# Kernel tuning notes

Measured on AMD Instinct MI355X. Metric: run time of the kernel, lower is better.

## Reference

```python
import jax, jax.numpy as jnp
import numpy as np

E = 8       # n_experts
K = 2       # k_experts
D_IN = 1024
D_OUT = 1024
D_EXP = 2048
N = 16384   # tokens (batch*seq, forward requires 2D input)


def setup_inputs() -> dict:
    key = jax.random.key(0)
    ks = jax.random.split(key, 4)
    x = jax.random.normal(ks[0], (N, D_IN), jnp.float32)
    Wg = jax.random.normal(ks[1], (E, D_IN), jnp.float32) * 0.02      # router weight
    bg = jnp.zeros((E,), jnp.float32)                                  # router bias
    W_in = jax.random.normal(ks[2], (E, D_EXP, D_IN), jnp.float32) * 0.02
    b_in = jnp.zeros((E, D_EXP), jnp.float32)                          # w_in_bias_init=0.0
    W_out = jax.random.normal(ks[3], (E, D_OUT, D_EXP), jnp.float32) * 0.02  # bias=False
    return {"x": x, "Wg": Wg, "bg": bg, "W_in": W_in, "b_in": b_in, "W_out": W_out}


def moe_forward(x, Wg, bg, W_in, b_in, W_out):
    # Eval mode: gate jitter / solu jitter / dropouts are training-only no-ops.
    n = x.shape[0]
    # --- routing ---
    logits = x @ Wg.T + bg                                 # [N, E]
    probs = jax.nn.softmax(logits, axis=-1)
    mean_probs = probs.mean(axis=0)                        # [E]
    k_vals, k_idx = jax.lax.top_k(probs, K)                # [N, K]
    k_w = k_vals / k_vals.sum(axis=-1, keepdims=True)      # renormalized gate weights
    counts = jnp.bincount(k_idx.reshape(-1), length=E)     # [E] int
    load_balancing_loss = E * jnp.sum((counts.astype(x.dtype) / n) * mean_probs)
    # --- dispatch + expert w_in (loop over fixed small E; combine with one-hot mask) ---
    sel = jax.nn.one_hot(k_idx, E, dtype=x.dtype)          # [N, K, E]
    h = jnp.zeros((n, K, D_EXP), x.dtype)                  # preacts per (token, slot)
    for e in range(E):
        he = x @ W_in[e].T + b_in[e]                       # [N, D_EXP]
        h = h + sel[:, :, e][..., None] * he[:, None, :]
    # --- SoLU (eval): softmax(preacts) * preacts over hidden dim ---
    acts = jax.nn.softmax(h, axis=-1) * h                  # [N, K, D_EXP]
    # --- expert w_out (no bias) ---
    out = jnp.zeros((n, K, D_OUT), x.dtype)
    for e in range(E):
        oe = jnp.einsum('nkh,oh->nko', acts, W_out[e])
        out = out + sel[:, :, e][..., None] * oe
    # --- weighted combine over the K chosen experts ---
    outputs = (out * k_w[..., None]).sum(axis=1)           # [N, D_OUT]
    return outputs, load_balancing_loss


def reference(x, Wg, bg, W_in, b_in, W_out):
    return moe_forward(x, Wg, bg, W_in, b_in, W_out)
```

## Files before the change

### kernel.cpp

```cpp
#include <hip/hip_runtime.h>
#include <hip/hip_bf16.h>
#include <stdint.h>

#define E_EXP 8
#define NTOK  16384
#define DIN   1024
#define DEXP  2048
#define DOUT  1024
#define NSLOT (NTOK*2)
#define MAXT  136

#define TS_T  (256*64)

typedef __attribute__((ext_vector_type(8))) short short8;
typedef __attribute__((ext_vector_type(8))) unsigned short ushort8;
typedef __attribute__((ext_vector_type(4))) unsigned short ushort4v;
typedef __attribute__((ext_vector_type(4))) float f32x4;

__device__ __forceinline__ unsigned short f2bf(float f){
  union { float f; uint32_t u; } v; v.f = f;
  uint32_t r = (v.u + 0x7FFFu + ((v.u >> 16) & 1u)) >> 16;
  return (unsigned short)r;
}
__device__ __forceinline__ float bf2f(unsigned short u){
  union { uint32_t u; float f; } v; v.u = ((uint32_t)u) << 16;
  return v.f;
}

__device__ __forceinline__ void async16(const void* g, void* l){
  __builtin_amdgcn_global_load_lds(
      (const __attribute__((address_space(1))) void*)g,
      (__attribute__((address_space(3))) void*)l, 16, 0, 0);
}

#define VMCNT8()  asm volatile("s_waitcnt vmcnt(8)"  ::: "memory")
#define VMCNT0()  asm volatile("s_waitcnt vmcnt(0)"  ::: "memory")
#define BARRIER() do { asm volatile("" ::: "memory"); __builtin_amdgcn_s_barrier(); asm volatile("" ::: "memory"); } while(0)

__global__ __launch_bounds__(256) void cast2(const float* __restrict__ a,
                                             const float* __restrict__ b,
                                             unsigned short* __restrict__ da,
                                             unsigned short* __restrict__ db,
                                             int na, int nb){
  int i = (blockIdx.x*256 + threadIdx.x)*8;
  const float* s; unsigned short* d;
  if (i < na){ s = a + i; d = da + i; }
  else { int j = i - na; if (j >= nb) return; s = b + j; d = db + j; }
  float4 x = *(const float4*)(s);
  float4 y = *(const float4*)(s+4);
  ushort8 o;
  o[0]=f2bf(x.x); o[1]=f2bf(x.y); o[2]=f2bf(x.z); o[3]=f2bf(x.w);
  o[4]=f2bf(y.x); o[5]=f2bf(y.y); o[6]=f2bf(y.z); o[7]=f2bf(y.w);
  *(ushort8*)d = o;
}

__global__ __launch_bounds__(256) void router(
    const float* __restrict__ x, const float* __restrict__ Wg, const float* __restrict__ bg,
    unsigned short* __restrict__ xb,
    int* __restrict__ eidx, float* __restrict__ gw,
    int* __restrict__ counts, float* __restrict__ probsum)
{
  __shared__ float sWg[E_EXP*DIN];
  __shared__ float sps[E_EXP];
  __shared__ int   scnt[E_EXP];
  const int tid = threadIdx.x;
  for (int i = tid; i < E_EXP*DIN; i += 256) sWg[i] = Wg[i];
  if (tid < E_EXP){ sps[tid]=0.f; scnt[tid]=0; }
  __syncthreads();
  const int lane = tid & 63;
  const int wv   = tid >> 6;
  for (int it = 0; it < 16; ++it){
    const int token = blockIdx.x*64 + wv*16 + it;
    float4 xv[4];
#pragma unroll
    for (int j=0;j<4;++j) xv[j] = *(const float4*)&x[(size_t)token*DIN + j*256 + lane*4];
#pragma unroll
    for (int j=0;j<4;++j){
      ushort4v o;
      o[0]=f2bf(xv[j].x); o[1]=f2bf(xv[j].y); o[2]=f2bf(xv[j].z); o[3]=f2bf(xv[j].w);
      *(ushort4v*)&xb[(size_t)token*DIN + j*256 + lane*4] = o;
    }
    float p[E_EXP];
#pragma unroll
    for (int e2=0;e2<E_EXP;++e2){
      float s = 0.f;
#pragma unroll
      for (int j=0;j<4;++j){
        const float4 w4 = *(const float4*)&sWg[e2*DIN + j*256 + lane*4];
        s += xv[j].x*w4.x + xv[j].y*w4.y + xv[j].z*w4.z + xv[j].w*w4.w;
      }
      p[e2] = s;
    }
#pragma unroll
    for (int d=1; d<64; d<<=1){
#pragma unroll
      for (int e2=0;e2<E_EXP;++e2) p[e2] += __shfl_xor(p[e2], d);
    }
    if (lane == 0){
      float mx = -1e30f;
#pragma unroll
      for (int e2=0;e2<E_EXP;++e2){ p[e2] += bg[e2]; mx = fmaxf(mx, p[e2]); }
      float se = 0.f;
#pragma unroll
      for (int e2=0;e2<E_EXP;++e2){ p[e2] = __expf(p[e2]-mx); se += p[e2]; }
      const float inv = 1.f/se;
#pragma unroll
      for (int e2=0;e2<E_EXP;++e2){ p[e2] *= inv; atomicAdd(&sps[e2], p[e2]); }
      int i1 = 0;
#pragma unroll
      for (int e2=1;e2<E_EXP;++e2) if (p[e2] > p[i1]) i1 = e2;
      int i2 = (i1==0) ? 1 : 0;
#pragma unroll
      for (int e2=0;e2<E_EXP;++e2) if (e2 != i1 && p[e2] > p[i2]) i2 = e2;
      const float v1 = p[i1], v2 = p[i2], s12 = v1 + v2;
      eidx[2*token]   = i1; eidx[2*token+1] = i2;
      gw[2*token]     = v1/s12; gw[2*token+1] = v2/s12;
      atomicAdd(&scnt[i1], 1); atomicAdd(&scnt[i2], 1);
    }
  }
  __syncthreads();
  if (tid < E_EXP){ atomicAdd(&counts[tid], scnt[tid]); atomicAdd(&probsum[tid], sps[tid]); }
}

__global__ void finalize(const int* __restrict__ counts, const float* __restrict__ probsum,
                         float* __restrict__ loss_out, int* __restrict__ offs,
                         int* __restrict__ cursor, int* __restrict__ tile_e,
                         int* __restrict__ tile_row, int* __restrict__ ntiles)
{
  const int lane = threadIdx.x;
  int c[E_EXP];
#pragma unroll
  for (int e=0;e<E_EXP;++e) c[e] = counts[e];
  int off[E_EXP+1], tb[E_EXP+1];
  off[0]=0; tb[0]=0;
#pragma unroll
  for (int e=0;e<E_EXP;++e){ off[e+1]=off[e]+c[e]; tb[e+1]=tb[e]+((c[e]+255)>>8); }
  if (lane==0){
    float loss=0.f;
#pragma unroll
    for (int e=0;e<E_EXP;++e) loss += (float)c[e]*probsum[e];
    *loss_out = loss * (8.f/((float)NTOK*(float)NTOK));
    *ntiles = tb[E_EXP];
    offs[E_EXP] = off[E_EXP];
  }
  if (lane < E_EXP){ cursor[lane]=0; offs[lane]=off[lane]; }
  const int nt = tb[E_EXP];
  for (int i=lane; i<nt; i+=64){
    int e=0;
#pragma unroll
    for (int k=0;k<E_EXP-1;++k) if (i >= tb[k+1]) e = k+1;
    tile_e[i]   = e;
    tile_row[i] = off[e] + (i - tb[e])*256;
  }
}

__global__ __launch_bounds__(256) void scatter(const int* __restrict__ eidx,
    const int* __restrict__ offs, int* __restrict__ cursor,
    int* __restrict__ ptok, int* __restrict__ inv)
{
  const int t = blockIdx.x*256 + threadIdx.x;
  if (t >= NTOK) return;
#pragma unroll
  for (int s=0;s<2;++s){
    const int e2  = eidx[2*t+s];
    const int pos = offs[e2] + atomicAdd(&cursor[e2], 1);
    ptok[pos] = t;
    inv[2*t+s] = pos;
  }
}

__global__ __launch_bounds__(512) void gemm1(
    const unsigned short* __restrict__ xb,
    const unsigned short* __restrict__ wib,
    const float* __restrict__ b_in,
    unsigned short* __restrict__ H,
    const int* __restrict__ ptok,
    const int* __restrict__ offs,
    const int* __restrict__ tile_e,
    const int* __restrict__ tile_row,
    const int* __restrict__ ntiles)
{
  const int gid   = (int)blockIdx.y * 8 + (int)blockIdx.x;
  const int rank  = (gid & 7) * 136 + (gid >> 3);
  const int rtile = rank >> 3;
  const int panel = rank & 7;
  if (rtile >= *ntiles) return;
  const int e    = tile_e[rtile];
  const int row0 = tile_row[rtile];
  const int seg_end = offs[e+1];
  const int col0 = panel * 256;

  __shared__ unsigned short As[2][TS_T];
  __shared__ unsigned short Bs[2][TS_T];

  const int tid  = threadIdx.x;
  const int lane = tid & 63;
  const int wv   = tid >> 6;
  const int wm   = wv >> 2;
  const int wn   = wv & 3;
  const int srow = tid >> 3;
  const int scol = ((tid & 7) ^ (srow & 7)) * 8;

  const unsigned short* ag[4];
#pragma unroll
  for (int i = 0; i < 4; ++i){
    int g = row0 + i*64 + srow; if (g > NSLOT-1) g = NSLOT-1;
    const int tok = ptok[g];
    ag[i] = xb + (size_t)tok*DIN + scol;
  }
  const unsigned short* bg4[4];
#pragma unroll
  for (int i = 0; i < 4; ++i)
    bg4[i] = wib + ((size_t)e*DEXP + col0 + i*64 + srow)*DIN + scol;
  float bias[4];
#pragma unroll
  for (int n = 0; n < 4; ++n)
    bias[n] = b_in[e*DEXP + col0 + wn*64 + n*16 + (lane&15)];

  f32x4 acc[8][4] = {};
  const int NK = DIN/64;
  int cur = 0;

  const unsigned int L0 = (wv*8)*64, L1 = (64+wv*8)*64, L2o = (128+wv*8)*64, L3 = (192+wv*8)*64;

  async16(ag[0],  &As[0][L0]);  async16(ag[1],  &As[0][L1]);
  async16(ag[2],  &As[0][L2o]); async16(ag[3],  &As[0][L3]);
  async16(bg4[0], &Bs[0][L0]);  async16(bg4[1], &Bs[0][L1]);
  async16(bg4[2], &Bs[0][L2o]); async16(bg4[3], &Bs[0][L3]);

  for (int kt = 0; kt < NK; ++kt){
    BARRIER();
    if (kt + 1 < NK){
      const int ko = (kt+1)*64;
      async16(ag[0]  + ko, &As[cur^1][L0]);  async16(ag[1]  + ko, &As[cur^1][L1]);
      async16(ag[2]  + ko, &As[cur^1][L2o]); async16(ag[3]  + ko, &As[cur^1][L3]);
      async16(bg4[0] + ko, &Bs[cur^1][L0]);  async16(bg4[1] + ko, &Bs[cur^1][L1]);
      async16(bg4[2] + ko, &Bs[cur^1][L2o]); async16(bg4[3] + ko, &Bs[cur^1][L3]);
      VMCNT8();
    } else {
      VMCNT0();
    }
    BARRIER();

    __builtin_amdgcn_s_setprio(1);
#pragma unroll
    for (int kk = 0; kk < 2; ++kk){
      const int ksl = ((kk*4 + (lane>>4)) ^ (lane & 7)) * 8;
      short8 a[8], b[4];
#pragma unroll
      for (int m = 0; m < 8; ++m)
        a[m] = *(const short8*)&As[cur][(wm*128 + m*16 + (lane&15))*64 + ksl];
#pragma unroll
      for (int n = 0; n < 4; ++n)
        b[n] = *(const short8*)&Bs[cur][(wn*64 + n*16 + (lane&15))*64 + ksl];
#pragma unroll
      for (int m = 0; m < 8; ++m)
#pragma unroll
        for (int n = 0; n < 4; ++n)
          acc[m][n] = __builtin_amdgcn_mfma_f32_16x16x32_bf16(a[m], b[n], acc[m][n], 0, 0, 0);
    }
    __builtin_amdgcn_s_setprio(0);
    cur ^= 1;
  }

#pragma unroll
  for (int m = 0; m < 8; ++m){
#pragma unroll
    for (int j = 0; j < 4; ++j){
      const int r = wm*128 + m*16 + (lane>>4)*4 + j;
      const int g = row0 + r;
      if (g < seg_end){
#pragma unroll
        for (int n = 0; n < 4; ++n){
          const int c = col0 + wn*64 + n*16 + (lane&15);
          H[(size_t)g*DEXP + c] = f2bf(acc[m][n][j] + bias[n]);
        }
      }
    }
  }
}

__global__ __launch_bounds__(256) void solu(unsigned short* __restrict__ H){
  const size_t row = blockIdx.x;
  unsigned short* hp = H + row*DEXP;
  const int tid  = threadIdx.x;
  const int lane = tid & 63;
  const int wv   = tid >> 6;
  const short8 hv = *(const short8*)&hp[tid*8];
  float f[8];
#pragma unroll
  for (int j=0;j<8;++j) f[j] = bf2f((unsigned short)hv[j]);
  float mx = f[0];
#pragma unroll
  for (int j=1;j<8;++j) mx = fmaxf(mx, f[j]);
  for (int d=1; d<64; d<<=1) mx = fmaxf(mx, __shfl_xor(mx, d));
  __shared__ float redm[4];
  __shared__ float reds[4];
  if (lane==0) redm[wv] = mx;
  __syncthreads();
  mx = fmaxf(fmaxf(redm[0],redm[1]), fmaxf(redm[2],redm[3]));
  float se = 0.f; float ex[8];
#pragma unroll
  for (int j=0;j<8;++j){ ex[j] = __expf(f[j]-mx); se += ex[j]; }
  for (int d=1; d<64; d<<=1) se += __shfl_xor(se, d);
  if (lane==0) reds[wv] = se;
  __syncthreads();
  se = reds[0]+reds[1]+reds[2]+reds[3];
  const float inv = 1.0f/se;
  ushort8 o;
#pragma unroll
  for (int j=0;j<8;++j) o[j] = f2bf(f[j]*ex[j]*inv);
  *(ushort8*)&hp[tid*8] = o;
}

__global__ __launch_bounds__(512) void gemm2(
    const unsigned short* __restrict__ ACT,
    const unsigned short* __restrict__ wob,
    unsigned short* __restrict__ Oslot,
    const int* __restrict__ offs,
    const int* __restrict__ tile_e,
    const int* __restrict__ tile_row,
    const int* __restrict__ ntiles)
{
  const int gid   = (int)blockIdx.y * 4 + (int)blockIdx.x;
  const int rank  = (gid & 7) * 68 + (gid >> 3);
  const int rtile = rank >> 2;
  const int panel = rank & 3;
  if (rtile >= *ntiles) return;
  const int e    = tile_e[rtile];
  const int row0 = tile_row[rtile];
  const int seg_end = offs[e+1];
  const int col0 = panel * 256;

  __shared__ unsigned short As[2][TS_T];
  __shared__ unsigned short Bs[2][TS_T];

  const int tid  = threadIdx.x;
  const int lane = tid & 63;
  const int wv   = tid >> 6;
  const int wm   = wv >> 2;
  const int wn   = wv & 3;
  const int srow = tid >> 3;
  const int scol = ((tid & 7) ^ (srow & 7)) * 8;

  const unsigned short* ag[4];
#pragma unroll
  for (int i = 0; i < 4; ++i){
    int g = row0 + i*64 + srow; if (g > NSLOT-1) g = NSLOT-1;
    ag[i] = ACT + (size_t)g*DEXP + scol;
  }
  const unsigned short* bg4[4];
#pragma unroll
  for (int i = 0; i < 4; ++i)
    bg4[i] = wob + ((size_t)e*DOUT + col0 + i*64 + srow)*DEXP + scol;

  f32x4 acc[8][4] = {};
  const int NK = DEXP/64;
  int cur = 0;

  const unsigned int L0 = (wv*8)*64, L1 = (64+wv*8)*64, L2o = (128+wv*8)*64, L3 = (192+wv*8)*64;

  async16(ag[0],  &As[0][L0]);  async16(ag[1],  &As[0][L1]);
  async16(ag[2],  &As[0][L2o]); async16(ag[3],  &As[0][L3]);
  async16(bg4[0], &Bs[0][L0]);  async16(bg4[1], &Bs[0][L1]);
  async16(bg4[2], &Bs[0][L2o]); async16(bg4[3], &Bs[0][L3]);

  for (int kt = 0; kt < NK; ++kt){
    BARRIER();
    if (kt + 1 < NK){
      const int ko = (kt+1)*64;
      async16(ag[0]  + ko, &As[cur^1][L0]);  async16(ag[1]  + ko, &As[cur^1][L1]);
      async16(ag[2]  + ko, &As[cur^1][L2o]); async16(ag[3]  + ko, &As[cur^1][L3]);
      async16(bg4[0] + ko, &Bs[cur^1][L0]);  async16(bg4[1] + ko, &Bs[cur^1][L1]);
      async16(bg4[2] + ko, &Bs[cur^1][L2o]); async16(bg4[3] + ko, &Bs[cur^1][L3]);
      VMCNT8();
    } else {
      VMCNT0();
    }
    BARRIER();

    __builtin_amdgcn_s_setprio(1);
#pragma unroll
    for (int kk = 0; kk < 2; ++kk){
      const int ksl = ((kk*4 + (lane>>4)) ^ (lane & 7)) * 8;
      short8 a[8], b[4];
#pragma unroll
      for (int m = 0; m < 8; ++m)
        a[m] = *(const short8*)&As[cur][(wm*128 + m*16 + (lane&15))*64 + ksl];
#pragma unroll
      for (int n = 0; n < 4; ++n)
        b[n] = *(const short8*)&Bs[cur][(wn*64 + n*16 + (lane&15))*64 + ksl];
#pragma unroll
      for (int m = 0; m < 8; ++m)
#pragma unroll
        for (int n = 0; n < 4; ++n)
          acc[m][n] = __builtin_amdgcn_mfma_f32_16x16x32_bf16(a[m], b[n], acc[m][n], 0, 0, 0);
    }
    __builtin_amdgcn_s_setprio(0);
    cur ^= 1;
  }

#pragma unroll
  for (int m = 0; m < 8; ++m){
#pragma unroll
    for (int j = 0; j < 4; ++j){
      const int r = wm*128 + m*16 + (lane>>4)*4 + j;
      const int g = row0 + r;
      if (g < seg_end){
#pragma unroll
        for (int n = 0; n < 4; ++n){
          const int c = col0 + wn*64 + n*16 + (lane&15);
          Oslot[(size_t)g*DOUT + c] = f2bf(acc[m][n][j]);
        }
      }
    }
  }
}

__global__ __launch_bounds__(256) void combine(const unsigned short* __restrict__ Oslot,
    const int* __restrict__ inv, const float* __restrict__ gw, float* __restrict__ out)
{
  const int t    = blockIdx.x*4 + (threadIdx.x >> 6);
  const int lane = threadIdx.x & 63;
  const int p0 = inv[2*t], p1 = inv[2*t+1];
  const float w0 = gw[2*t], w1 = gw[2*t+1];
  const unsigned short* r0 = Oslot + (size_t)p0*DOUT + lane*16;
  const unsigned short* r1 = Oslot + (size_t)p1*DOUT + lane*16;
  ushort8 a0 = *(const ushort8*)r0;
  ushort8 a1 = *(const ushort8*)(r0 + 8);
  ushort8 b0 = *(const ushort8*)r1;
  ushort8 b1 = *(const ushort8*)(r1 + 8);
  float* op = out + (size_t)t*DOUT + lane*16;
  float4 o;
#pragma unroll
  for (int q = 0; q < 2; ++q){
    const ushort8 ua = q ? a1 : a0;
    const ushort8 ub = q ? b1 : b0;
#pragma unroll
    for (int h = 0; h < 2; ++h){
      o.x = w0*bf2f(ua[h*4+0]) + w1*bf2f(ub[h*4+0]);
      o.y = w0*bf2f(ua[h*4+1]) + w1*bf2f(ub[h*4+1]);
      o.z = w0*bf2f(ua[h*4+2]) + w1*bf2f(ub[h*4+2]);
      o.w = w0*bf2f(ua[h*4+3]) + w1*bf2f(ub[h*4+3]);
      *(float4*)(op + q*8 + h*4) = o;
    }
  }
}

extern "C" void kernel_launch(void* const* d_in, const int* in_sizes, int n_in,
                              void* d_out, int out_size, void* d_ws, size_t ws_size,
                              hipStream_t stream)
{
  const float* x     = (const float*)d_in[0];
  const float* Wg    = (const float*)d_in[1];
  const float* bgp   = (const float*)d_in[2];
  const float* W_in  = (const float*)d_in[3];
  const float* b_in  = (const float*)d_in[4];
  const float* W_out = (const float*)d_in[5];
  float* out = (float*)d_out;

  char* base = (char*)d_ws;
  size_t o = 0;
  unsigned short* xb  = (unsigned short*)(base + o); o += (size_t)NTOK*DIN*2;
  unsigned short* wib = (unsigned short*)(base + o); o += (size_t)E_EXP*DEXP*DIN*2;
  unsigned short* wob = (unsigned short*)(base + o); o += (size_t)E_EXP*DOUT*DEXP*2;
  unsigned short* H   = (unsigned short*)(base + o); o += (size_t)NSLOT*DEXP*2;
  unsigned short* Oslot = (unsigned short*)d_ws;
  int*   eidx    = (int*)(base + o);   o += (size_t)NSLOT*4;
  float* gw      = (float*)(base + o); o += (size_t)NSLOT*4;
  int*   ptok    = (int*)(base + o);   o += (size_t)NSLOT*4;
  int*   inv     = (int*)(base + o);   o += (size_t)NSLOT*4;
  int*   counts  = (int*)(base + o);   o += 32;
  float* probsum = (float*)(base + o); o += 32;
  int*   cursor  = (int*)(base + o);   o += 32;
  int*   offs    = (int*)(base + o);   o += 64;
  int*   tile_e  = (int*)(base + o);   o += (size_t)MAXT*4;
  int*   tile_row= (int*)(base + o);   o += (size_t)MAXT*4;
  int*   ntiles  = (int*)(base + o);   o += 64;

  hipMemsetAsync(counts, 0, 96, stream);

  cast2<<<dim3(16384), 256, 0, stream>>>(W_in, W_out, wib, wob,
                                         E_EXP*DEXP*DIN, E_EXP*DOUT*DEXP);

  router<<<dim3(256), 256, 0, stream>>>(x, Wg, bgp, xb, eidx, gw, counts, probsum);
  finalize<<<dim3(1), 64, 0, stream>>>(counts, probsum, out + (size_t)NTOK*DOUT,
                                       offs, cursor, tile_e, tile_row, ntiles);
  scatter<<<dim3(64), 256, 0, stream>>>(eidx, offs, cursor, ptok, inv);

  gemm1<<<dim3(DEXP/256, MAXT), 512, 0, stream>>>(xb, wib, b_in, H, ptok, offs,
                                                  tile_e, tile_row, ntiles);
  solu<<<dim3(NSLOT), 256, 0, stream>>>(H);
  gemm2<<<dim3(DOUT/256, MAXT), 512, 0, stream>>>(H, wob, Oslot, offs,
                                                  tile_e, tile_row, ntiles);
  combine<<<dim3(NTOK/4), 256, 0, stream>>>(Oslot, inv, gw, out);
}
```

Baseline: 739.4 us.

## Fuse gated combine into gemm2 via atomic adds and halve GEMM K-tile

The combine kernel and the bf16 Oslot intermediate are removed. gemm2 now scales each result row by its gate weight and atomically adds it into the zeroed fp32 output row of the owning token, and scatter writes per-slot gate weights in expert-sorted order. Both GEMMs also drop the K tile from 64 to 32, which halves LDS use per stage, changes the swizzle and doubles the number of barrier iterations. The atomic float adds make the summation order nondeterministic and add atomic traffic, and the smaller K tile may raise the share of time spent on synchronisation.

```diff
diff --git a/kernel.cpp b/kernel.cpp
--- a/kernel.cpp
+++ b/kernel.cpp
@@ -10,7 +10,7 @@
 #define NSLOT (NTOK*2)
 #define MAXT  136
 
-#define TS_T  (256*64)
+#define TS_T  (256*32)
 
 typedef __attribute__((ext_vector_type(8))) short short8;
 typedef __attribute__((ext_vector_type(8))) unsigned short ushort8;
@@ -33,7 +33,7 @@
       (__attribute__((address_space(3))) void*)l, 16, 0, 0);
 }
 
-#define VMCNT8()  asm volatile("s_waitcnt vmcnt(8)"  ::: "memory")
+#define VMCNT4()  asm volatile("s_waitcnt vmcnt(4)"  ::: "memory")
 #define VMCNT0()  asm volatile("s_waitcnt vmcnt(0)"  ::: "memory")
 #define BARRIER() do { asm volatile("" ::: "memory"); __builtin_amdgcn_s_barrier(); asm volatile("" ::: "memory"); } while(0)
 
@@ -155,8 +155,9 @@
 }
 
 __global__ __launch_bounds__(256) void scatter(const int* __restrict__ eidx,
+    const float* __restrict__ gw,
     const int* __restrict__ offs, int* __restrict__ cursor,
-    int* __restrict__ ptok, int* __restrict__ inv)
+    int* __restrict__ ptok, float* __restrict__ pw)
 {
   const int t = blockIdx.x*256 + threadIdx.x;
   if (t >= NTOK) return;
@@ -165,7 +166,7 @@
     const int e2  = eidx[2*t+s];
     const int pos = offs[e2] + atomicAdd(&cursor[e2], 1);
     ptok[pos] = t;
-    inv[2*t+s] = pos;
+    pw[pos]   = gw[2*t+s];
   }
 }
 
@@ -198,61 +199,56 @@
   const int wv   = tid >> 6;
   const int wm   = wv >> 2;
   const int wn   = wv & 3;
-  const int srow = tid >> 3;
-  const int scol = ((tid & 7) ^ (srow & 7)) * 8;
-
-  const unsigned short* ag[4];
-#pragma unroll
-  for (int i = 0; i < 4; ++i){
-    int g = row0 + i*64 + srow; if (g > NSLOT-1) g = NSLOT-1;
+  const int srow = tid >> 2;
+  const int sgr  = ((tid & 3) ^ ((tid >> 3) & 3)) * 8;
+
+  const unsigned short* ag[2];
+#pragma unroll
+  for (int i = 0; i < 2; ++i){
+    int g = row0 + i*128 + srow; if (g > NSLOT-1) g = NSLOT-1;
     const int tok = ptok[g];
-    ag[i] = xb + (size_t)tok*DIN + scol;
-  }
-  const unsigned short* bg4[4];
-#pragma unroll
-  for (int i = 0; i < 4; ++i)
-    bg4[i] = wib + ((size_t)e*DEXP + col0 + i*64 + srow)*DIN + scol;
+    ag[i] = xb + (size_t)tok*DIN + sgr;
+  }
+  const unsigned short* bg2[2];
+#pragma unroll
+  for (int i = 0; i < 2; ++i)
+    bg2[i] = wib + ((size_t)e*DEXP + col0 + i*128 + srow)*DIN + sgr;
   float bias[4];
 #pragma unroll
   for (int n = 0; n < 4; ++n)
     bias[n] = b_in[e*DEXP + col0 + wn*64 + n*16 + (lane&15)];
 
   f32x4 acc[8][4] = {};
-  const int NK = DIN/64;
+  const int NK = DIN/32;
   int cur = 0;
 
-  const unsigned int L0 = (wv*8)*64, L1 = (64+wv*8)*64, L2o = (128+wv*8)*64, L3 = (192+wv*8)*64;
-
-  async16(ag[0],  &As[0][L0]);  async16(ag[1],  &As[0][L1]);
-  async16(ag[2],  &As[0][L2o]); async16(ag[3],  &As[0][L3]);
-  async16(bg4[0], &Bs[0][L0]);  async16(bg4[1], &Bs[0][L1]);
-  async16(bg4[2], &Bs[0][L2o]); async16(bg4[3], &Bs[0][L3]);
+  const unsigned int Ld = tid*8;
+  const int rsl = (((lane>>4) ^ ((lane>>1)&3)) * 8);
+
+  async16(ag[0],  &As[0][Ld]);          async16(ag[1],  &As[0][128*32 + Ld]);
+  async16(bg2[0], &Bs[0][Ld]);          async16(bg2[1], &Bs[0][128*32 + Ld]);
 
   for (int kt = 0; kt < NK; ++kt){
     BARRIER();
     if (kt + 1 < NK){
-      const int ko = (kt+1)*64;
-      async16(ag[0]  + ko, &As[cur^1][L0]);  async16(ag[1]  + ko, &As[cur^1][L1]);
-      async16(ag[2]  + ko, &As[cur^1][L2o]); async16(ag[3]  + ko, &As[cur^1][L3]);
-      async16(bg4[0] + ko, &Bs[cur^1][L0]);  async16(bg4[1] + ko, &Bs[cur^1][L1]);
-      async16(bg4[2] + ko, &Bs[cur^1][L2o]); async16(bg4[3] + ko, &Bs[cur^1][L3]);
-      VMCNT8();
+      const int ko = (kt+1)*32;
+      async16(ag[0]  + ko, &As[cur^1][Ld]);  async16(ag[1]  + ko, &As[cur^1][128*32 + Ld]);
+      async16(bg2[0] + ko, &Bs[cur^1][Ld]);  async16(bg2[1] + ko, &Bs[cur^1][128*32 + Ld]);
+      VMCNT4();
     } else {
       VMCNT0();
     }
     BARRIER();
 
     __builtin_amdgcn_s_setprio(1);
-#pragma unroll
-    for (int kk = 0; kk < 2; ++kk){
-      const int ksl = ((kk*4 + (lane>>4)) ^ (lane & 7)) * 8;
+    {
       short8 a[8], b[4];
 #pragma unroll
       for (int m = 0; m < 8; ++m)
-        a[m] = *(const short8*)&As[cur][(wm*128 + m*16 + (lane&15))*64 + ksl];
+        a[m] = *(const short8*)&As[cur][(wm*128 + m*16 + (lane&15))*32 + rsl];
 #pragma unroll
       for (int n = 0; n < 4; ++n)
-        b[n] = *(const short8*)&Bs[cur][(wn*64 + n*16 + (lane&15))*64 + ksl];
+        b[n] = *(const short8*)&Bs[cur][(wn*64 + n*16 + (lane&15))*32 + rsl];
 #pragma unroll
       for (int m = 0; m < 8; ++m)
 #pragma unroll
@@ -316,7 +312,9 @@
 __global__ __launch_bounds__(512) void gemm2(
     const unsigned short* __restrict__ ACT,
     const unsigned short* __restrict__ wob,
-    unsigned short* __restrict__ Oslot,
+    float* __restrict__ out,
+    const int* __restrict__ ptok,
+    const float* __restrict__ pw,
     const int* __restrict__ offs,
     const int* __restrict__ tile_e,
     const int* __restrict__ tile_row,
@@ -340,56 +338,51 @@
   const int wv   = tid >> 6;
   const int wm   = wv >> 2;
   const int wn   = wv & 3;
-  const int srow = tid >> 3;
-  const int scol = ((tid & 7) ^ (srow & 7)) * 8;
-
-  const unsigned short* ag[4];
-#pragma unroll
-  for (int i = 0; i < 4; ++i){
-    int g = row0 + i*64 + srow; if (g > NSLOT-1) g = NSLOT-1;
-    ag[i] = ACT + (size_t)g*DEXP + scol;
-  }
-  const unsigned short* bg4[4];
-#pragma unroll
-  for (int i = 0; i < 4; ++i)
-    bg4[i] = wob + ((size_t)e*DOUT + col0 + i*64 + srow)*DEXP + scol;
+  const int srow = tid >> 2;
+  const int sgr  = ((tid & 3) ^ ((tid >> 3) & 3)) * 8;
+
+  const unsigned short* ag[2];
+#pragma unroll
+  for (int i = 0; i < 2; ++i){
+    int g = row0 + i*128 + srow; if (g > NSLOT-1) g = NSLOT-1;
+    ag[i] = ACT + (size_t)g*DEXP + sgr;
+  }
+  const unsigned short* bg2[2];
+#pragma unroll
+  for (int i = 0; i < 2; ++i)
+    bg2[i] = wob + ((size_t)e*DOUT + col0 + i*128 + srow)*DEXP + sgr;
 
   f32x4 acc[8][4] = {};
-  const int NK = DEXP/64;
+  const int NK = DEXP/32;
   int cur = 0;
 
-  const unsigned int L0 = (wv*8)*64, L1 = (64+wv*8)*64, L2o = (128+wv*8)*64, L3 = (192+wv*8)*64;
-
-  async16(ag[0],  &As[0][L0]);  async16(ag[1],  &As[0][L1]);
-  async16(ag[2],  &As[0][L2o]); async16(ag[3],  &As[0][L3]);
-  async16(bg4[0], &Bs[0][L0]);  async16(bg4[1], &Bs[0][L1]);
-  async16(bg4[2], &Bs[0][L2o]); async16(bg4[3], &Bs[0][L3]);
+  const unsigned int Ld = tid*8;
+  const int rsl = (((lane>>4) ^ ((lane>>1)&3)) * 8);
+
+  async16(ag[0],  &As[0][Ld]);          async16(ag[1],  &As[0][128*32 + Ld]);
+  async16(bg2[0], &Bs[0][Ld]);          async16(bg2[1], &Bs[0][128*32 + Ld]);
 
   for (int kt = 0; kt < NK; ++kt){
     BARRIER();
     if (kt + 1 < NK){
-      const int ko = (kt+1)*64;
-      async16(ag[0]  + ko, &As[cur^1][L0]);  async16(ag[1]  + ko, &As[cur^1][L1]);
-      async16(ag[2]  + ko, &As[cur^1][L2o]); async16(ag[3]  + ko, &As[cur^1][L3]);
-      async16(bg4[0] + ko, &Bs[cur^1][L0]);  async16(bg4[1] + ko, &Bs[cur^1][L1]);
-      async16(bg4[2] + ko, &Bs[cur^1][L2o]); async16(bg4[3] + ko, &Bs[cur^1][L3]);
-      VMCNT8();
+      const int ko = (kt+1)*32;
+      async16(ag[0]  + ko, &As[cur^1][Ld]);  async16(ag[1]  + ko, &As[cur^1][128*32 + Ld]);
+      async16(bg2[0] + ko, &Bs[cur^1][Ld]);  async16(bg2[1] + ko, &Bs[cur^1][128*32 + Ld]);
+      VMCNT4();
     } else {
       VMCNT0();
     }
     BARRIER();
 
     __builtin_amdgcn_s_setprio(1);
-#pragma unroll
-    for (int kk = 0; kk < 2; ++kk){
-      const int ksl = ((kk*4 + (lane>>4)) ^ (lane & 7)) * 8;
+    {
       short8 a[8], b[4];
 #pragma unroll
       for (int m = 0; m < 8; ++m)
-        a[m] = *(const short8*)&As[cur][(wm*128 + m*16 + (lane&15))*64 + ksl];
+        a[m] = *(const short8*)&As[cur][(wm*128 + m*16 + (lane&15))*32 + rsl];
 #pragma unroll
       for (int n = 0; n < 4; ++n)
-        b[n] = *(const short8*)&Bs[cur][(wn*64 + n*16 + (lane&15))*64 + ksl];
+        b[n] = *(const short8*)&Bs[cur][(wn*64 + n*16 + (lane&15))*32 + rsl];
 #pragma unroll
       for (int m = 0; m < 8; ++m)
 #pragma unroll
@@ -407,42 +400,15 @@
       const int r = wm*128 + m*16 + (lane>>4)*4 + j;
       const int g = row0 + r;
       if (g < seg_end){
+        const int tok   = ptok[g];
+        const float wgt = pw[g];
+        float* op = out + (size_t)tok*DOUT;
 #pragma unroll
         for (int n = 0; n < 4; ++n){
           const int c = col0 + wn*64 + n*16 + (lane&15);
-          Oslot[(size_t)g*DOUT + c] = f2bf(acc[m][n][j]);
+          unsafeAtomicAdd(op + c, wgt * acc[m][n][j]);
         }
       }
-    }
-  }
-}
-
-__global__ __launch_bounds__(256) void combine(const unsigned short* __restrict__ Oslot,
-    const int* __restrict__ inv, const float* __restrict__ gw, float* __restrict__ out)
-{
-  const int t    = blockIdx.x*4 + (threadIdx.x >> 6);
-  const int lane = threadIdx.x & 63;
-  const int p0 = inv[2*t], p1 = inv[2*t+1];
-  const float w0 = gw[2*t], w1 = gw[2*t+1];
-  const unsigned short* r0 = Oslot + (size_t)p0*DOUT + lane*16;
-  const unsigned short* r1 = Oslot + (size_t)p1*DOUT + lane*16;
-  ushort8 a0 = *(const ushort8*)r0;
-  ushort8 a1 = *(const ushort8*)(r0 + 8);
-  ushort8 b0 = *(const ushort8*)r1;
-  ushort8 b1 = *(const ushort8*)(r1 + 8);
-  float* op = out + (size_t)t*DOUT + lane*16;
-  float4 o;
-#pragma unroll
-  for (int q = 0; q < 2; ++q){
-    const ushort8 ua = q ? a1 : a0;
-    const ushort8 ub = q ? b1 : b0;
-#pragma unroll
-    for (int h = 0; h < 2; ++h){
-      o.x = w0*bf2f(ua[h*4+0]) + w1*bf2f(ub[h*4+0]);
-      o.y = w0*bf2f(ua[h*4+1]) + w1*bf2f(ub[h*4+1]);
-      o.z = w0*bf2f(ua[h*4+2]) + w1*bf2f(ub[h*4+2]);
-      o.w = w0*bf2f(ua[h*4+3]) + w1*bf2f(ub[h*4+3]);
-      *(float4*)(op + q*8 + h*4) = o;
     }
   }
 }
@@ -465,11 +431,10 @@
   unsigned short* wib = (unsigned short*)(base + o); o += (size_t)E_EXP*DEXP*DIN*2;
   unsigned short* wob = (unsigned short*)(base + o); o += (size_t)E_EXP*DOUT*DEXP*2;
   unsigned short* H   = (unsigned short*)(base + o); o += (size_t)NSLOT*DEXP*2;
-  unsigned short* Oslot = (unsigned short*)d_ws;
   int*   eidx    = (int*)(base + o);   o += (size_t)NSLOT*4;
   float* gw      = (float*)(base + o); o += (size_t)NSLOT*4;
   int*   ptok    = (int*)(base + o);   o += (size_t)NSLOT*4;
-  int*   inv     = (int*)(base + o);   o += (size_t)NSLOT*4;
+  float* pw      = (float*)(base + o); o += (size_t)NSLOT*4;
   int*   counts  = (int*)(base + o);   o += 32;
   float* probsum = (float*)(base + o); o += 32;
   int*   cursor  = (int*)(base + o);   o += 32;
@@ -478,6 +443,7 @@
   int*   tile_row= (int*)(base + o);   o += (size_t)MAXT*4;
   int*   ntiles  = (int*)(base + o);   o += 64;
 
+  hipMemsetAsync(d_out, 0, (size_t)NTOK*DOUT*4 + 4, stream);
   hipMemsetAsync(counts, 0, 96, stream);
 
   cast2<<<dim3(16384), 256, 0, stream>>>(W_in, W_out, wib, wob,
@@ -486,12 +452,11 @@
   router<<<dim3(256), 256, 0, stream>>>(x, Wg, bgp, xb, eidx, gw, counts, probsum);
   finalize<<<dim3(1), 64, 0, stream>>>(counts, probsum, out + (size_t)NTOK*DOUT,
                                        offs, cursor, tile_e, tile_row, ntiles);
-  scatter<<<dim3(64), 256, 0, stream>>>(eidx, offs, cursor, ptok, inv);
+  scatter<<<dim3(64), 256, 0, stream>>>(eidx, gw, offs, cursor, ptok, pw);
 
   gemm1<<<dim3(DEXP/256, MAXT), 512, 0, stream>>>(xb, wib, b_in, H, ptok, offs,
                                                   tile_e, tile_row, ntiles);
   solu<<<dim3(NSLOT), 256, 0, stream>>>(H);
-  gemm2<<<dim3(DOUT/256, MAXT), 512, 0, stream>>>(H, wob, Oslot, offs,
+  gemm2<<<dim3(DOUT/256, MAXT), 512, 0, stream>>>(H, wob, out, ptok, pw, offs,
                                                   tile_e, tile_row, ntiles);
-  combine<<<dim3(NTOK/4), 256, 0, stream>>>(Oslot, inv, gw, out);
-}
+}
```

After: 865.8 us. +17.1%, slower.

## Fuse weighted combine into gemm2 epilogue via atomic adds; restructure K-loop sync

Applied to the files above, without the earlier changes.

The gate-weighted combine kernel and the bf16 Oslot intermediate are removed. gemm2 now scales each output by the slot's gate weight, which scatter writes into a new per-slot array, and atomically adds it into the zeroed fp32 output at the token's row. The GEMM K-loops also move the wait and barrier to after the MFMA block, so each iteration issues the next tile's loads first and then waits for all outstanding loads. In exchange the output needs a memset plus fp32 atomics, the summation order becomes nondeterministic, and the prefetch no longer overlaps the wait as it did with the partial vmcnt.

```diff
diff --git a/kernel.cpp b/kernel.cpp
--- a/kernel.cpp
+++ b/kernel.cpp
@@ -33,7 +33,6 @@
       (__attribute__((address_space(3))) void*)l, 16, 0, 0);
 }
 
-#define VMCNT8()  asm volatile("s_waitcnt vmcnt(8)"  ::: "memory")
 #define VMCNT0()  asm volatile("s_waitcnt vmcnt(0)"  ::: "memory")
 #define BARRIER() do { asm volatile("" ::: "memory"); __builtin_amdgcn_s_barrier(); asm volatile("" ::: "memory"); } while(0)
 
@@ -155,8 +154,9 @@
 }
 
 __global__ __launch_bounds__(256) void scatter(const int* __restrict__ eidx,
+    const float* __restrict__ gw,
     const int* __restrict__ offs, int* __restrict__ cursor,
-    int* __restrict__ ptok, int* __restrict__ inv)
+    int* __restrict__ ptok, float* __restrict__ pw)
 {
   const int t = blockIdx.x*256 + threadIdx.x;
   if (t >= NTOK) return;
@@ -165,9 +165,15 @@
     const int e2  = eidx[2*t+s];
     const int pos = offs[e2] + atomicAdd(&cursor[e2], 1);
     ptok[pos] = t;
-    inv[2*t+s] = pos;
-  }
-}
+    pw[pos]   = gw[2*t+s];
+  }
+}
+
+#define STAGE8(buf, ko) do {                                              \
+  async16(ag[0]+(ko),  &As[buf][L0]);  async16(ag[1]+(ko),  &As[buf][L1]);\
+  async16(ag[2]+(ko),  &As[buf][L2o]); async16(ag[3]+(ko),  &As[buf][L3]);\
+  async16(bg4[0]+(ko), &Bs[buf][L0]);  async16(bg4[1]+(ko), &Bs[buf][L1]);\
+  async16(bg4[2]+(ko), &Bs[buf][L2o]); async16(bg4[3]+(ko), &Bs[buf][L3]);} while(0)
 
 __global__ __launch_bounds__(512) void gemm1(
     const unsigned short* __restrict__ xb,
@@ -223,24 +229,12 @@
 
   const unsigned int L0 = (wv*8)*64, L1 = (64+wv*8)*64, L2o = (128+wv*8)*64, L3 = (192+wv*8)*64;
 
-  async16(ag[0],  &As[0][L0]);  async16(ag[1],  &As[0][L1]);
-  async16(ag[2],  &As[0][L2o]); async16(ag[3],  &As[0][L3]);
-  async16(bg4[0], &Bs[0][L0]);  async16(bg4[1], &Bs[0][L1]);
-  async16(bg4[2], &Bs[0][L2o]); async16(bg4[3], &Bs[0][L3]);
+  STAGE8(0, 0);
+  VMCNT0();
+  BARRIER();
 
   for (int kt = 0; kt < NK; ++kt){
-    BARRIER();
-    if (kt + 1 < NK){
-      const int ko = (kt+1)*64;
-      async16(ag[0]  + ko, &As[cur^1][L0]);  async16(ag[1]  + ko, &As[cur^1][L1]);
-      async16(ag[2]  + ko, &As[cur^1][L2o]); async16(ag[3]  + ko, &As[cur^1][L3]);
-      async16(bg4[0] + ko, &Bs[cur^1][L0]);  async16(bg4[1] + ko, &Bs[cur^1][L1]);
-      async16(bg4[2] + ko, &Bs[cur^1][L2o]); async16(bg4[3] + ko, &Bs[cur^1][L3]);
-      VMCNT8();
-    } else {
-      VMCNT0();
-    }
-    BARRIER();
+    if (kt + 1 < NK) STAGE8(cur^1, (kt+1)*64);
 
     __builtin_amdgcn_s_setprio(1);
 #pragma unroll
@@ -260,6 +254,9 @@
           acc[m][n] = __builtin_amdgcn_mfma_f32_16x16x32_bf16(a[m], b[n], acc[m][n], 0, 0, 0);
     }
     __builtin_amdgcn_s_setprio(0);
+
+    VMCNT0();
+    BARRIER();
     cur ^= 1;
   }
 
@@ -316,7 +313,9 @@
 __global__ __launch_bounds__(512) void gemm2(
     const unsigned short* __restrict__ ACT,
     const unsigned short* __restrict__ wob,
-    unsigned short* __restrict__ Oslot,
+    float* __restrict__ out,
+    const int* __restrict__ ptok,
+    const float* __restrict__ pw,
     const int* __restrict__ offs,
     const int* __restrict__ tile_e,
     const int* __restrict__ tile_row,
@@ -360,24 +359,12 @@
 
   const unsigned int L0 = (wv*8)*64, L1 = (64+wv*8)*64, L2o = (128+wv*8)*64, L3 = (192+wv*8)*64;
 
-  async16(ag[0],  &As[0][L0]);  async16(ag[1],  &As[0][L1]);
-  async16(ag[2],  &As[0][L2o]); async16(ag[3],  &As[0][L3]);
-  async16(bg4[0], &Bs[0][L0]);  async16(bg4[1], &Bs[0][L1]);
-  async16(bg4[2], &Bs[0][L2o]); async16(bg4[3], &Bs[0][L3]);
+  STAGE8(0, 0);
+  VMCNT0();
+  BARRIER();
 
   for (int kt = 0; kt < NK; ++kt){
-    BARRIER();
-    if (kt + 1 < NK){
-      const int ko = (kt+1)*64;
-      async16(ag[0]  + ko, &As[cur^1][L0]);  async16(ag[1]  + ko, &As[cur^1][L1]);
-      async16(ag[2]  + ko, &As[cur^1][L2o]); async16(ag[3]  + ko, &As[cur^1][L3]);
-      async16(bg4[0] + ko, &Bs[cur^1][L0]);  async16(bg4[1] + ko, &Bs[cur^1][L1]);
-      async16(bg4[2] + ko, &Bs[cur^1][L2o]); async16(bg4[3] + ko, &Bs[cur^1][L3]);
-      VMCNT8();
-    } else {
-      VMCNT0();
-    }
-    BARRIER();
+    if (kt + 1 < NK) STAGE8(cur^1, (kt+1)*64);
 
     __builtin_amdgcn_s_setprio(1);
 #pragma unroll
@@ -397,6 +384,9 @@
           acc[m][n] = __builtin_amdgcn_mfma_f32_16x16x32_bf16(a[m], b[n], acc[m][n], 0, 0, 0);
     }
     __builtin_amdgcn_s_setprio(0);
+
+    VMCNT0();
+    BARRIER();
     cur ^= 1;
   }
 
@@ -407,42 +397,15 @@
       const int r = wm*128 + m*16 + (lane>>4)*4 + j;
       const int g = row0 + r;
       if (g < seg_end){
+        const int tok   = ptok[g];
+        const float wgt = pw[g];
+        float* op = out + (size_t)tok*DOUT;
 #pragma unroll
         for (int n = 0; n < 4; ++n){
           const int c = col0 + wn*64 + n*16 + (lane&15);
-          Oslot[(size_t)g*DOUT + c] = f2bf(acc[m][n][j]);
+          unsafeAtomicAdd(op + c, wgt * acc[m][n][j]);
         }
       }
-    }
-  }
-}
-
-__global__ __launch_bounds__(256) void combine(const unsigned short* __restrict__ Oslot,
-    const int* __restrict__ inv, const float* __restrict__ gw, float* __restrict__ out)
-{
-  const int t    = blockIdx.x*4 + (threadIdx.x >> 6);
-  const int lane = threadIdx.x & 63;
-  const int p0 = inv[2*t], p1 = inv[2*t+1];
-  const float w0 = gw[2*t], w1 = gw[2*t+1];
-  const unsigned short* r0 = Oslot + (size_t)p0*DOUT + lane*16;
-  const unsigned short* r1 = Oslot + (size_t)p1*DOUT + lane*16;
-  ushort8 a0 = *(const ushort8*)r0;
-  ushort8 a1 = *(const ushort8*)(r0 + 8);
-  ushort8 b0 = *(const ushort8*)r1;
-  ushort8 b1 = *(const ushort8*)(r1 + 8);
-  float* op = out + (size_t)t*DOUT + lane*16;
-  float4 o;
-#pragma unroll
-  for (int q = 0; q < 2; ++q){
-    const ushort8 ua = q ? a1 : a0;
-    const ushort8 ub = q ? b1 : b0;
-#pragma unroll
-    for (int h = 0; h < 2; ++h){
-      o.x = w0*bf2f(ua[h*4+0]) + w1*bf2f(ub[h*4+0]);
-      o.y = w0*bf2f(ua[h*4+1]) + w1*bf2f(ub[h*4+1]);
-      o.z = w0*bf2f(ua[h*4+2]) + w1*bf2f(ub[h*4+2]);
-      o.w = w0*bf2f(ua[h*4+3]) + w1*bf2f(ub[h*4+3]);
-      *(float4*)(op + q*8 + h*4) = o;
     }
   }
 }
@@ -465,11 +428,10 @@
   unsigned short* wib = (unsigned short*)(base + o); o += (size_t)E_EXP*DEXP*DIN*2;
   unsigned short* wob = (unsigned short*)(base + o); o += (size_t)E_EXP*DOUT*DEXP*2;
   unsigned short* H   = (unsigned short*)(base + o); o += (size_t)NSLOT*DEXP*2;
-  unsigned short* Oslot = (unsigned short*)d_ws;
   int*   eidx    = (int*)(base + o);   o += (size_t)NSLOT*4;
   float* gw      = (float*)(base + o); o += (size_t)NSLOT*4;
   int*   ptok    = (int*)(base + o);   o += (size_t)NSLOT*4;
-  int*   inv     = (int*)(base + o);   o += (size_t)NSLOT*4;
+  float* pw      = (float*)(base + o); o += (size_t)NSLOT*4;
   int*   counts  = (int*)(base + o);   o += 32;
   float* probsum = (float*)(base + o); o += 32;
   int*   cursor  = (int*)(base + o);   o += 32;
@@ -478,6 +440,7 @@
   int*   tile_row= (int*)(base + o);   o += (size_t)MAXT*4;
   int*   ntiles  = (int*)(base + o);   o += 64;
 
+  hipMemsetAsync(d_out, 0, (size_t)NTOK*DOUT*4 + 4, stream);
   hipMemsetAsync(counts, 0, 96, stream);
 
   cast2<<<dim3(16384), 256, 0, stream>>>(W_in, W_out, wib, wob,
@@ -486,12 +449,11 @@
   router<<<dim3(256), 256, 0, stream>>>(x, Wg, bgp, xb, eidx, gw, counts, probsum);
   finalize<<<dim3(1), 64, 0, stream>>>(counts, probsum, out + (size_t)NTOK*DOUT,
                                        offs, cursor, tile_e, tile_row, ntiles);
-  scatter<<<dim3(64), 256, 0, stream>>>(eidx, offs, cursor, ptok, inv);
+  scatter<<<dim3(64), 256, 0, stream>>>(eidx, gw, offs, cursor, ptok, pw);
 
   gemm1<<<dim3(DEXP/256, MAXT), 512, 0, stream>>>(xb, wib, b_in, H, ptok, offs,
                                                   tile_e, tile_row, ntiles);
   solu<<<dim3(NSLOT), 256, 0, stream>>>(H);
-  gemm2<<<dim3(DOUT/256, MAXT), 512, 0, stream>>>(H, wob, Oslot, offs,
+  gemm2<<<dim3(DOUT/256, MAXT), 512, 0, stream>>>(H, wob, out, ptok, pw, offs,
                                                   tile_e, tile_row, ntiles);
-  combine<<<dim3(NTOK/4), 256, 0, stream>>>(Oslot, inv, gw, out);
-}
+}
```

After: 805.7 us. 1.09x slower.
